# Performance work log

Hardware: AMD Instinct MI355X
Metric: run time of the kernel (lower is better)

## Reference

```python
import jax, jax.numpy as jnp
import numpy as np

DIM = 768
HEAD_DIM = 64          # num_head arg (per-head dim)
N_HEADS = DIM // HEAD_DIM  # 12
B, N = 4, 2048


def setup_inputs() -> dict:
    key = jax.random.key(0)
    ks = jax.random.split(key, 7)
    s = DIM ** -0.5
    return {
        "x":  jax.random.normal(ks[0], (B, N, DIM), jnp.float32),
        "wq": jax.random.normal(ks[1], (DIM, DIM), jnp.float32) * s,
        "bq": jax.random.normal(ks[2], (DIM,), jnp.float32) * 0.01,
        "wk": jax.random.normal(ks[3], (DIM, DIM), jnp.float32) * s,
        "bk": jax.random.normal(ks[4], (DIM,), jnp.float32) * 0.01,
        "wv": jax.random.normal(ks[5], (DIM, DIM), jnp.float32) * s,
        "bv": jax.random.normal(ks[6], (DIM,), jnp.float32) * 0.01,
    }


def reference(x, wq, bq, wk, bk, wv, bv):
    # torch Linear: y = x @ W.T + b
    q = x @ wq.T + bq
    k = x @ wk.T + bk
    v = x @ wv.T + bv
    # split heads: b n (h d) -> b h n d
    def split(t):
        return t.reshape(B, N, N_HEADS, HEAD_DIM).transpose(0, 2, 1, 3)
    q, k, v = split(q), split(k), split(v)
    scale = HEAD_DIM ** -0.5
    logit = jnp.einsum("bhnd,bhmd->bhnm", q, k) * scale  # [B,H,N,N]
    attn = jax.nn.softmax(logit, axis=-1)
    out = jnp.einsum("bhnm,bhmd->bhnd", attn, v)
    # concat heads: b h n d -> b n (h d)
    return out.transpose(0, 2, 1, 3).reshape(B, N, DIM)
```

## Files before the change

kernel.cpp:

```cpp
#include <hip/hip_runtime.h>
#include <cstdint>

#define NSEQ 2048
#define DIM  768
#define NH   12
#define HD   64

typedef __attribute__((ext_vector_type(8))) short bf16x8;
typedef __attribute__((ext_vector_type(4))) float f32x4;
typedef unsigned short u16;

#define MFMA16(a,b,c) __builtin_amdgcn_mfma_f32_16x16x32_bf16(a,b,c,0,0,0)

#define QSCALE 0.1803368801111204f

__device__ __forceinline__ u16 f2bf(float f){
  unsigned u = __builtin_bit_cast(unsigned, f);
  return (u16)((u + 0x7fffu + ((u >> 16) & 1u)) >> 16);
}
__device__ __forceinline__ u16 f2bf_ru(float f){
  unsigned u = __builtin_bit_cast(unsigned, f);
  return (u16)((u + 0x8000u) >> 16);
}

typedef __attribute__((address_space(1))) void gvoid_t;
typedef __attribute__((address_space(3))) void lvoid_t;
__device__ __forceinline__ void g2l16(const void* g, void* l){
  __builtin_amdgcn_global_load_lds((gvoid_t*)g, (lvoid_t*)l, 16, 0, 0);
}

__global__ __launch_bounds__(256) void convert_all(
    const float* __restrict__ x,  const float* __restrict__ wq,
    const float* __restrict__ wk, const float* __restrict__ wv,
    u16* __restrict__ xb, u16* __restrict__ wb){
  int blk = blockIdx.x, tid = threadIdx.x;
  const float* src; u16* dst; long idx;
  if (blk < 6144){ src = x; dst = xb; idx = (long)blk*256 + tid; }
  else {
    int r = blk - 6144; int s = r / 576; r -= s*576;
    src = (s==0) ? wq : (s==1) ? wk : wv;
    dst = wb + (long)s * (768*768);
    idx = (long)r*256 + tid;
  }
  float4 v = ((const float4*)src)[idx];
  ushort4 o;
  o.x = f2bf(v.x); o.y = f2bf(v.y); o.z = f2bf(v.z); o.w = f2bf(v.w);
  ((ushort4*)dst)[idx] = o;
}

__global__ __launch_bounds__(256,3) void qkv_gemm(
    const u16* __restrict__ xb, const u16* __restrict__ wb,
    const float* __restrict__ bq, const float* __restrict__ bk,
    const float* __restrict__ bv,
    u16* __restrict__ Qo, u16* __restrict__ Ko, u16* __restrict__ Vo){
  __shared__ __align__(16) u16 ldsX[128*64];
  __shared__ __align__(16) u16 ldsW[128*64];
  int tid  = threadIdx.x;
  int w    = tid >> 6, lane = tid & 63;
  int xcd  = blockIdx.x & 7, j = blockIdx.x >> 3;
  int bm   = xcd*8 + j/18, bn = j%18;
  int wm   = w >> 1, wn = w & 1;
  int l15  = lane & 15, g = lane >> 4;
  int srow = lane >> 3;
  int scol = ((lane & 7) ^ srow) * 8;

  const u16* xg = xb + (long)bm*128*768;
  const u16* wg = wb + (long)bn*128*768;

  f32x4 acc[4][4] = {};

  for (int k0 = 0; k0 < 768; k0 += 64){
    if (k0) __syncthreads();
    #pragma unroll
    for (int jj = 0; jj < 4; jj++){
      int rr = (w*4 + jj)*8 + srow;
      g2l16(xg + (long)rr*768 + k0 + scol, &ldsX[(w*4 + jj)*512]);
      g2l16(wg + (long)rr*768 + k0 + scol, &ldsW[(w*4 + jj)*512]);
    }
    __syncthreads();
    #pragma unroll
    for (int ks = 0; ks < 2; ks++){
      bf16x8 af[4], bfr[4];
      #pragma unroll
      for (int im = 0; im < 4; im++){
        int row = wm*64 + im*16 + l15;
        af[im] = *(const bf16x8*)&ldsX[row*64 + (((ks*4 + g) ^ (row & 7))*8)];
      }
      #pragma unroll
      for (int in = 0; in < 4; in++){
        int row = wn*64 + in*16 + l15;
        bfr[in] = *(const bf16x8*)&ldsW[row*64 + (((ks*4 + g) ^ (row & 7))*8)];
      }
      #pragma unroll
      for (int im = 0; im < 4; im++)
        #pragma unroll
        for (int in = 0; in < 4; in++)
          acc[im][in] = MFMA16(af[im], bfr[in], acc[im][in]);
    }
  }

  int seg = bn / 6;
  const float* bias = (seg==0) ? bq : (seg==1) ? bk : bv;
  #pragma unroll
  for (int in = 0; in < 4; in++){
    int o  = bn*128 + wn*64 + in*16 + l15;
    int oo = o - seg*768;
    int h  = oo >> 6, d = oo & 63;
    float bb = bias[oo];
    #pragma unroll
    for (int im = 0; im < 4; im++){
      int t  = bm*128 + wm*64 + im*16 + g*4;
      int bi = t >> 11, n0 = t & 2047;
      f32x4 a = acc[im][in];
      if (seg == 2){
        ushort4 pk;
        pk.x = f2bf(a[0] + bb); pk.y = f2bf(a[1] + bb);
        pk.z = f2bf(a[2] + bb); pk.w = f2bf(a[3] + bb);
        *(ushort4*)&Vo[((long)(bi*NH + h)*HD + d)*NSEQ + n0] = pk;
      } else if (seg == 0){
        #pragma unroll
        for (int r = 0; r < 4; r++)
          Qo[((long)(bi*NH + h)*NSEQ + n0 + r)*HD + d] = f2bf((a[r] + bb)*QSCALE);
      } else {
        #pragma unroll
        for (int r = 0; r < 4; r++)
          Ko[((long)(bi*NH + h)*NSEQ + n0 + r)*HD + d] = f2bf(a[r] + bb);
      }
    }
  }
}

__global__ __launch_bounds__(256,3) void attn(
    const u16* __restrict__ Q, const u16* __restrict__ K,
    const u16* __restrict__ VT, float* __restrict__ out){
  __shared__ __align__(16) u16 kls[2][64*64];
  __shared__ __align__(16) u16 vls[2][64*64];
  __shared__ __align__(16) u16 pls[4][2][32*36];
  int tid = threadIdx.x;
  int w   = tid >> 6, lane = tid & 63;
  int xcd = blockIdx.x & 7, j = blockIdx.x >> 3;
  int bh  = xcd*6 + (j >> 4), qc = j & 15;
  int b   = bh / NH, h = bh - b*NH;
  int l15 = lane & 15, g = lane >> 4;
  int srow = lane >> 3;
  int scol = ((lane & 7) ^ srow) * 8;

  const u16* Qb = Q  + (long)bh*NSEQ*HD;
  const u16* Kb = K  + (long)bh*NSEQ*HD;
  const u16* Vb = VT + (long)bh*HD*NSEQ;

  bf16x8 qf[2][2];
  #pragma unroll
  for (int in = 0; in < 2; in++)
    #pragma unroll
    for (int ks = 0; ks < 2; ks++)
      qf[in][ks] = *(const bf16x8*)
        &Qb[(long)(qc*128 + w*32 + in*16 + l15)*HD + ks*32 + g*8];

  f32x4 oa[4][2] = {};
  float ls[2] = {0.f, 0.f};

#define STAGE(c0, bf)                                                         \
  {                                                                           \
    _Pragma("unroll")                                                         \
    for (int jj = 0; jj < 2; jj++){                                           \
      int rr = jj*32 + w*8;                                                   \
      g2l16(Kb + (long)((c0) + rr + srow)*HD + scol,  &kls[bf][rr*64]);       \
      g2l16(Vb + (long)(rr + srow)*NSEQ + (c0) + scol, &vls[bf][rr*64]);      \
    }                                                                         \
  }

#define HALF(bf, hh)                                                          \
  {                                                                           \
    u16* pbuf = &pls[w][hh][0];                                               \
    bf16x8 kf[2][2];                                                          \
    _Pragma("unroll")                                                         \
    for (int cm = 0; cm < 2; cm++){                                           \
      int rr = (hh*2 + cm)*16 + l15;                                          \
      _Pragma("unroll")                                                       \
      for (int ks = 0; ks < 2; ks++)                                          \
        kf[cm][ks] = *(const bf16x8*)&kls[bf][rr*64 + (((ks*4+g)^(rr&7))*8)]; \
    }                                                                         \
    f32x4 T[2][2];                                                            \
    _Pragma("unroll")                                                         \
    for (int cm = 0; cm < 2; cm++)                                            \
      _Pragma("unroll")                                                       \
      for (int in = 0; in < 2; in++){                                         \
        f32x4 t = {0.f,0.f,0.f,0.f};                                          \
        t = MFMA16(kf[cm][0], qf[in][0], t);                                  \
        t = MFMA16(kf[cm][1], qf[in][1], t);                                  \
        T[cm][in] = t;                                                        \
      }                                                                       \
    _Pragma("unroll")                                                         \
    for (int in = 0; in < 2; in++){                                           \
      float s = 0.f;                                                          \
      _Pragma("unroll")                                                       \
      for (int cm = 0; cm < 2; cm++){                                         \
        float p0 = __builtin_amdgcn_exp2f(T[cm][in][0]);                      \
        float p1 = __builtin_amdgcn_exp2f(T[cm][in][1]);                      \
        float p2 = __builtin_amdgcn_exp2f(T[cm][in][2]);                      \
        float p3 = __builtin_amdgcn_exp2f(T[cm][in][3]);                      \
        s += (p0 + p1) + (p2 + p3);                                           \
        ushort4 pk;                                                           \
        pk.x = f2bf_ru(p0); pk.y = f2bf_ru(p1);                               \
        pk.z = f2bf_ru(p2); pk.w = f2bf_ru(p3);                               \
        *(ushort4*)&pbuf[(in*16 + l15)*36 + cm*16 + g*4] = pk;                \
      }                                                                       \
      ls[in] += s;                                                            \
    }                                                                         \
    bf16x8 pf[2], vf[4];                                                      \
    _Pragma("unroll")                                                         \
    for (int in = 0; in < 2; in++)                                            \
      pf[in] = *(const bf16x8*)&pbuf[(in*16 + l15)*36 + g*8];                 \
    _Pragma("unroll")                                                         \
    for (int dm = 0; dm < 4; dm++){                                           \
      int rr = dm*16 + l15;                                                   \
      vf[dm] = *(const bf16x8*)&vls[bf][rr*64 + (((hh*4+g)^(rr&7))*8)];       \
    }                                                                         \
    _Pragma("unroll")                                                         \
    for (int dm = 0; dm < 4; dm++)                                            \
      _Pragma("unroll")                                                       \
      for (int in = 0; in < 2; in++)                                          \
        oa[dm][in] = MFMA16(vf[dm], pf[in], oa[dm][in]);                      \
  }

  STAGE(0, 0);
  __syncthreads();
  for (int i = 0; i < 32; i++){
    int cb = i & 1, nb = cb ^ 1;
    STAGE(((i+1) & 31)*64, nb);
    HALF(cb, 0);
    HALF(cb, 1);
    __syncthreads();
  }
#undef STAGE
#undef HALF

  #pragma unroll
  for (int in = 0; in < 2; in++){
    ls[in] += __shfl_xor(ls[in], 16);
    ls[in] += __shfl_xor(ls[in], 32);
  }
  #pragma unroll
  for (int in = 0; in < 2; in++){
    float inv = 1.f / ls[in];
    int r = qc*128 + w*32 + in*16 + l15;
    #pragma unroll
    for (int dm = 0; dm < 4; dm++){
      f32x4 v = oa[dm][in];
      v *= inv;
      int d = dm*16 + g*4;
      *(f32x4*)&out[(long)(b*NSEQ + r)*DIM + h*HD + d] = v;
    }
  }
}

extern "C" void kernel_launch(void* const* d_in, const int* in_sizes, int n_in,
                              void* d_out, int out_size, void* d_ws, size_t ws_size,
                              hipStream_t stream){
  (void)in_sizes; (void)n_in; (void)out_size; (void)ws_size;
  const float* x  = (const float*)d_in[0];
  const float* wq = (const float*)d_in[1];
  const float* bq = (const float*)d_in[2];
  const float* wk = (const float*)d_in[3];
  const float* bk = (const float*)d_in[4];
  const float* wv = (const float*)d_in[5];
  const float* bv = (const float*)d_in[6];

  char* ws = (char*)d_ws;
  u16* xb = (u16*)ws;
  u16* wb = (u16*)(ws + 12582912);
  u16* Qp = (u16*)(ws + 16121856);
  u16* Kp = (u16*)(ws + 28704768);
  u16* Vp = (u16*)(ws + 41287680);

  convert_all<<<7872, 256, 0, stream>>>(x, wq, wk, wv, xb, wb);
  qkv_gemm<<<1152, 256, 0, stream>>>(xb, wb, bq, bk, bv, Qp, Kp, Vp);
  attn<<<768, 256, 0, stream>>>(Qp, Kp, Vp, (float*)d_out);
}
```

Baseline: 213.2 us.

## Use 32x32 MFMA in attention with register-shuffled P, vectorize QK epilogue

The attention kernel switches from 16x16x32 to 32x32x16 bf16 MFMA tiles, so each wave covers 32 query rows with one accumulator set. The P tile stays in registers, with a cross-half shuffle repacking it into the operand layout, which removes the per-wave LDS round trip for probabilities and the LDS it used. The occupancy hint rises from 3 to 4 blocks per CU. In the QKV GEMM, Q/K tiles swap MFMA operand order so each lane holds 4 contiguous head-dim outputs, allowing vectorized float4 bias loads and 8-byte stores instead of scattered 2-byte stores.

```diff
diff --git a/kernel.cpp b/kernel.cpp
--- a/kernel.cpp
+++ b/kernel.cpp
@@ -6,11 +6,14 @@
 #define NH   12
 #define HD   64
 
-typedef __attribute__((ext_vector_type(8))) short bf16x8;
-typedef __attribute__((ext_vector_type(4))) float f32x4;
+typedef __attribute__((ext_vector_type(8)))  short bf16x8;
+typedef __attribute__((ext_vector_type(4)))  float f32x4;
+typedef __attribute__((ext_vector_type(16))) float f32x16;
+typedef __attribute__((ext_vector_type(4)))  int   i32x4;
 typedef unsigned short u16;
 
 #define MFMA16(a,b,c) __builtin_amdgcn_mfma_f32_16x16x32_bf16(a,b,c,0,0,0)
+#define MFMA32(a,b,c) __builtin_amdgcn_mfma_f32_32x32x16_bf16(a,b,c,0,0,0)
 
 #define QSCALE 0.1803368801111204f
 
@@ -18,9 +21,10 @@
   unsigned u = __builtin_bit_cast(unsigned, f);
   return (u16)((u + 0x7fffu + ((u >> 16) & 1u)) >> 16);
 }
-__device__ __forceinline__ u16 f2bf_ru(float f){
-  unsigned u = __builtin_bit_cast(unsigned, f);
-  return (u16)((u + 0x8000u) >> 16);
+__device__ __forceinline__ int pk2bf(float a, float b){
+  unsigned ua = (__builtin_bit_cast(unsigned, a) + 0x8000u) >> 16;
+  unsigned ub = (__builtin_bit_cast(unsigned, b) + 0x8000u) & 0xffff0000u;
+  return (int)(ua | ub);
 }
 
 typedef __attribute__((address_space(1))) void gvoid_t;
@@ -63,6 +67,8 @@
   int l15  = lane & 15, g = lane >> 4;
   int srow = lane >> 3;
   int scol = ((lane & 7) ^ srow) * 8;
+  int seg  = bn / 6;
+  bool isv = (seg == 2);
 
   const u16* xg = xb + (long)bm*128*768;
   const u16* wg = wb + (long)bn*128*768;
@@ -91,57 +97,74 @@
         int row = wn*64 + in*16 + l15;
         bfr[in] = *(const bf16x8*)&ldsW[row*64 + (((ks*4 + g) ^ (row & 7))*8)];
       }
-      #pragma unroll
-      for (int im = 0; im < 4; im++)
+      if (isv){
         #pragma unroll
-        for (int in = 0; in < 4; in++)
-          acc[im][in] = MFMA16(af[im], bfr[in], acc[im][in]);
-    }
-  }
-
-  int seg = bn / 6;
+        for (int im = 0; im < 4; im++)
+          #pragma unroll
+          for (int in = 0; in < 4; in++)
+            acc[im][in] = MFMA16(af[im], bfr[in], acc[im][in]);
+      } else {
+        #pragma unroll
+        for (int im = 0; im < 4; im++)
+          #pragma unroll
+          for (int in = 0; in < 4; in++)
+            acc[im][in] = MFMA16(bfr[in], af[im], acc[im][in]);
+      }
+    }
+  }
+
   const float* bias = (seg==0) ? bq : (seg==1) ? bk : bv;
-  #pragma unroll
-  for (int in = 0; in < 4; in++){
-    int o  = bn*128 + wn*64 + in*16 + l15;
-    int oo = o - seg*768;
-    int h  = oo >> 6, d = oo & 63;
-    float bb = bias[oo];
-    #pragma unroll
-    for (int im = 0; im < 4; im++){
-      int t  = bm*128 + wm*64 + im*16 + g*4;
-      int bi = t >> 11, n0 = t & 2047;
-      f32x4 a = acc[im][in];
-      if (seg == 2){
+  if (isv){
+    #pragma unroll
+    for (int in = 0; in < 4; in++){
+      int o  = bn*128 + wn*64 + in*16 + l15;
+      int oo = o - 2*768;
+      int h  = oo >> 6, d = oo & 63;
+      float bb = bias[oo];
+      #pragma unroll
+      for (int im = 0; im < 4; im++){
+        int t  = bm*128 + wm*64 + im*16 + g*4;
+        int bi = t >> 11, n0 = t & 2047;
+        f32x4 a = acc[im][in];
         ushort4 pk;
         pk.x = f2bf(a[0] + bb); pk.y = f2bf(a[1] + bb);
         pk.z = f2bf(a[2] + bb); pk.w = f2bf(a[3] + bb);
         *(ushort4*)&Vo[((long)(bi*NH + h)*HD + d)*NSEQ + n0] = pk;
-      } else if (seg == 0){
-        #pragma unroll
-        for (int r = 0; r < 4; r++)
-          Qo[((long)(bi*NH + h)*NSEQ + n0 + r)*HD + d] = f2bf((a[r] + bb)*QSCALE);
-      } else {
-        #pragma unroll
-        for (int r = 0; r < 4; r++)
-          Ko[((long)(bi*NH + h)*NSEQ + n0 + r)*HD + d] = f2bf(a[r] + bb);
-      }
-    }
-  }
-}
-
-__global__ __launch_bounds__(256,3) void attn(
+      }
+    }
+  } else {
+    u16* dst = (seg==0) ? Qo : Ko;
+    float sc = (seg==0) ? QSCALE : 1.0f;
+    #pragma unroll
+    for (int im = 0; im < 4; im++){
+      int t  = bm*128 + wm*64 + im*16 + l15;
+      int bi = t >> 11, n0 = t & 2047;
+      #pragma unroll
+      for (int in = 0; in < 4; in++){
+        int oo = bn*128 + wn*64 + in*16 + g*4 - seg*768;
+        int h  = oo >> 6, d0 = oo & 63;
+        float4 bb = *(const float4*)&bias[oo];
+        f32x4 a = acc[im][in];
+        ushort4 pk;
+        pk.x = f2bf((a[0] + bb.x)*sc); pk.y = f2bf((a[1] + bb.y)*sc);
+        pk.z = f2bf((a[2] + bb.z)*sc); pk.w = f2bf((a[3] + bb.w)*sc);
+        *(ushort4*)&dst[((long)(bi*NH + h)*NSEQ + n0)*HD + d0] = pk;
+      }
+    }
+  }
+}
+
+__global__ __launch_bounds__(256,4) void attn(
     const u16* __restrict__ Q, const u16* __restrict__ K,
     const u16* __restrict__ VT, float* __restrict__ out){
   __shared__ __align__(16) u16 kls[2][64*64];
   __shared__ __align__(16) u16 vls[2][64*64];
-  __shared__ __align__(16) u16 pls[4][2][32*36];
   int tid = threadIdx.x;
   int w   = tid >> 6, lane = tid & 63;
   int xcd = blockIdx.x & 7, j = blockIdx.x >> 3;
   int bh  = xcd*6 + (j >> 4), qc = j & 15;
   int b   = bh / NH, h = bh - b*NH;
-  int l15 = lane & 15, g = lane >> 4;
+  int l31 = lane & 31, hi = lane >> 5;
   int srow = lane >> 3;
   int scol = ((lane & 7) ^ srow) * 8;
 
@@ -149,16 +172,17 @@
   const u16* Kb = K  + (long)bh*NSEQ*HD;
   const u16* Vb = VT + (long)bh*HD*NSEQ;
 
-  bf16x8 qf[2][2];
-  #pragma unroll
-  for (int in = 0; in < 2; in++)
-    #pragma unroll
-    for (int ks = 0; ks < 2; ks++)
-      qf[in][ks] = *(const bf16x8*)
-        &Qb[(long)(qc*128 + w*32 + in*16 + l15)*HD + ks*32 + g*8];
-
-  f32x4 oa[4][2] = {};
-  float ls[2] = {0.f, 0.f};
+  int r0 = qc*128 + w*32;
+  bf16x8 qf[4];
+  {
+    const u16* qrow = Qb + (long)(r0 + l31)*HD;
+    #pragma unroll
+    for (int dk = 0; dk < 4; dk++)
+      qf[dk] = *(const bf16x8*)&qrow[dk*16 + hi*8];
+  }
+
+  f32x16 oa[2] = {};
+  float ls = 0.f;
 
 #define STAGE(c0, bf)                                                         \
   {                                                                           \
@@ -170,58 +194,47 @@
     }                                                                         \
   }
 
-#define HALF(bf, hh)                                                          \
+#define KH(bf, kh)                                                            \
   {                                                                           \
-    u16* pbuf = &pls[w][hh][0];                                               \
-    bf16x8 kf[2][2];                                                          \
-    _Pragma("unroll")                                                         \
-    for (int cm = 0; cm < 2; cm++){                                           \
-      int rr = (hh*2 + cm)*16 + l15;                                          \
+    bf16x8 kf[4];                                                             \
+    _Pragma("unroll")                                                         \
+    for (int dk = 0; dk < 4; dk++)                                            \
+      kf[dk] = *(const bf16x8*)                                               \
+        &kls[bf][((kh)*32 + l31)*64 + (((dk*2 + hi) ^ (l31 & 7))*8)];         \
+    f32x16 T = {};                                                            \
+    _Pragma("unroll")                                                         \
+    for (int dk = 0; dk < 4; dk++)                                            \
+      T = MFMA32(kf[dk], qf[dk], T);                                          \
+    int PD[4][2];                                                             \
+    _Pragma("unroll")                                                         \
+    for (int q = 0; q < 4; q++){                                              \
+      float p0 = __builtin_amdgcn_exp2f(T[q*4+0]);                            \
+      float p1 = __builtin_amdgcn_exp2f(T[q*4+1]);                            \
+      float p2 = __builtin_amdgcn_exp2f(T[q*4+2]);                            \
+      float p3 = __builtin_amdgcn_exp2f(T[q*4+3]);                            \
+      ls += (p0 + p1) + (p2 + p3);                                            \
+      PD[q][0] = pk2bf(p0, p1);                                               \
+      PD[q][1] = pk2bf(p2, p3);                                               \
+    }                                                                         \
+    _Pragma("unroll")                                                         \
+    for (int kc = 0; kc < 2; kc++){                                           \
+      int s0 = hi ? PD[2*kc][0] : PD[2*kc+1][0];                              \
+      int s1 = hi ? PD[2*kc][1] : PD[2*kc+1][1];                              \
+      int x0 = __shfl_xor(s0, 32);                                            \
+      int x1 = __shfl_xor(s1, 32);                                            \
+      i32x4 pr;                                                               \
+      pr[0] = hi ? x0 : PD[2*kc][0];                                          \
+      pr[1] = hi ? x1 : PD[2*kc][1];                                          \
+      pr[2] = hi ? PD[2*kc+1][0] : x0;                                        \
+      pr[3] = hi ? PD[2*kc+1][1] : x1;                                        \
+      bf16x8 pf = __builtin_bit_cast(bf16x8, pr);                             \
       _Pragma("unroll")                                                       \
-      for (int ks = 0; ks < 2; ks++)                                          \
-        kf[cm][ks] = *(const bf16x8*)&kls[bf][rr*64 + (((ks*4+g)^(rr&7))*8)]; \
+      for (int dt = 0; dt < 2; dt++){                                         \
+        bf16x8 vf = *(const bf16x8*)                                          \
+          &vls[bf][(dt*32 + l31)*64 + ((((kh)*4 + kc*2 + hi) ^ (l31 & 7))*8)];\
+        oa[dt] = MFMA32(vf, pf, oa[dt]);                                      \
+      }                                                                       \
     }                                                                         \
-    f32x4 T[2][2];                                                            \
-    _Pragma("unroll")                                                         \
-    for (int cm = 0; cm < 2; cm++)                                            \
-      _Pragma("unroll")                                                       \
-      for (int in = 0; in < 2; in++){                                         \
-        f32x4 t = {0.f,0.f,0.f,0.f};                                          \
-        t = MFMA16(kf[cm][0], qf[in][0], t);                                  \
-        t = MFMA16(kf[cm][1], qf[in][1], t);                                  \
-        T[cm][in] = t;                                                        \
-      }                                                                       \
-    _Pragma("unroll")                                                         \
-    for (int in = 0; in < 2; in++){                                           \
-      float s = 0.f;                                                          \
-      _Pragma("unroll")                                                       \
-      for (int cm = 0; cm < 2; cm++){                                         \
-        float p0 = __builtin_amdgcn_exp2f(T[cm][in][0]);                      \
-        float p1 = __builtin_amdgcn_exp2f(T[cm][in][1]);                      \
-        float p2 = __builtin_amdgcn_exp2f(T[cm][in][2]);                      \
-        float p3 = __builtin_amdgcn_exp2f(T[cm][in][3]);                      \
-        s += (p0 + p1) + (p2 + p3);                                           \
-        ushort4 pk;                                                           \
-        pk.x = f2bf_ru(p0); pk.y = f2bf_ru(p1);                               \
-        pk.z = f2bf_ru(p2); pk.w = f2bf_ru(p3);                               \
-        *(ushort4*)&pbuf[(in*16 + l15)*36 + cm*16 + g*4] = pk;                \
-      }                                                                       \
-      ls[in] += s;                                                            \
-    }                                                                         \
-    bf16x8 pf[2], vf[4];                                                      \
-    _Pragma("unroll")                                                         \
-    for (int in = 0; in < 2; in++)                                            \
-      pf[in] = *(const bf16x8*)&pbuf[(in*16 + l15)*36 + g*8];                 \
-    _Pragma("unroll")                                                         \
-    for (int dm = 0; dm < 4; dm++){                                           \
-      int rr = dm*16 + l15;                                                   \
-      vf[dm] = *(const bf16x8*)&vls[bf][rr*64 + (((hh*4+g)^(rr&7))*8)];       \
-    }                                                                         \
-    _Pragma("unroll")                                                         \
-    for (int dm = 0; dm < 4; dm++)                                            \
-      _Pragma("unroll")                                                       \
-      for (int in = 0; in < 2; in++)                                          \
-        oa[dm][in] = MFMA16(vf[dm], pf[in], oa[dm][in]);                      \
   }
 
   STAGE(0, 0);
@@ -229,30 +242,27 @@
   for (int i = 0; i < 32; i++){
     int cb = i & 1, nb = cb ^ 1;
     STAGE(((i+1) & 31)*64, nb);
-    HALF(cb, 0);
-    HALF(cb, 1);
+    KH(cb, 0);
+    KH(cb, 1);
     __syncthreads();
   }
 #undef STAGE
-#undef HALF
-
+#undef KH
+
+  ls += __shfl_xor(ls, 32);
+  float inv = 1.f / ls;
+
+  float* op = &out[(long)(b*NSEQ + r0 + l31)*DIM + h*HD];
   #pragma unroll
-  for (int in = 0; in < 2; in++){
-    ls[in] += __shfl_xor(ls[in], 16);
-    ls[in] += __shfl_xor(ls[in], 32);
-  }
-  #pragma unroll
-  for (int in = 0; in < 2; in++){
-    float inv = 1.f / ls[in];
-    int r = qc*128 + w*32 + in*16 + l15;
-    #pragma unroll
-    for (int dm = 0; dm < 4; dm++){
-      f32x4 v = oa[dm][in];
+  for (int dt = 0; dt < 2; dt++)
+    #pragma unroll
+    for (int rq = 0; rq < 4; rq++){
+      f32x4 v;
+      v[0] = oa[dt][rq*4+0]; v[1] = oa[dt][rq*4+1];
+      v[2] = oa[dt][rq*4+2]; v[3] = oa[dt][rq*4+3];
       v *= inv;
-      int d = dm*16 + g*4;
-      *(f32x4*)&out[(long)(b*NSEQ + r)*DIM + h*HD + d] = v;
-    }
-  }
+      *(f32x4*)&op[dt*32 + rq*8 + hi*4] = v;
+    }
 }
 
 extern "C" void kernel_launch(void* const* d_in, const int* in_sizes, int n_in,
```

After: 275.6 us. +29.3%, slower.
